# Performance work log

Hardware: AMD Instinct MI355X
Metric: run time of the kernel (lower is better)

## Reference

```python
import jax, jax.numpy as jnp
import numpy as np

N_NODES = 50000
N_EDGES = 1000000
NODE_F = 64
EDGE_F = 64
OUT_F = 128
K = 2  # matches init k=2


def setup_inputs() -> dict:
    key = jax.random.key(0)
    k1, k2, k3, k4, k5, k6 = jax.random.split(key, 6)
    node_feat = jax.random.normal(k1, (N_NODES, NODE_F), dtype=jnp.float32)
    edge_feat = jax.random.normal(k2, (N_EDGES, EDGE_F), dtype=jnp.float32)
    # nn.Linear(edge_feats*2 + node_feats, out_feats): weight [out, in], bias [out]
    W = jax.random.normal(k3, (OUT_F, 2 * EDGE_F + NODE_F), dtype=jnp.float32) * 0.05
    b = jax.random.normal(k4, (OUT_F,), dtype=jnp.float32) * 0.05
    src = jax.random.randint(k5, (N_EDGES,), 0, N_NODES, dtype=jnp.int64)
    dst = jax.random.randint(k6, (N_EDGES,), 0, N_NODES, dtype=jnp.int64)
    return {"node_feat": node_feat, "edge_feat": edge_feat, "W": W, "b": b,
            "src": src, "dst": dst}


def reference(node_feat, edge_feat, W, b, src, dst):
    N = node_feat.shape[0]
    # norm = in_degrees().clamp(min=1) ** -0.5, shape [N, 1]
    deg = jax.ops.segment_sum(jnp.ones_like(dst, dtype=node_feat.dtype), dst,
                              num_segments=N)
    norm = jnp.maximum(deg, 1.0) ** -0.5
    norm = norm[:, None]
    # DGL semantics: update_all(copy_e, sum) overwrites ndata['h'] with the
    # scatter-sum of edge data over destination nodes; apply_edges then copies
    # the (un-normalized) node 'h' back to edges via edge.src.
    e = edge_feat  # [E, EDGE_F]
    fstack = [node_feat]
    for _ in range(K):
        h = jax.ops.segment_sum(e, dst, num_segments=N)  # [N, EDGE_F]
        fstack.append(h * norm)
        e = h[src]  # apply_edges: e = src node h (un-normalized)
    rst = jnp.concatenate(fstack, axis=-1) @ W.T + b  # [N, OUT_F]
    est = rst[src]  # final apply_edges copies lin output to edges
    return rst, est
```

## Files before the change

### kernel.cpp

```cpp
#include <hip/hip_runtime.h>
#include <hip/hip_bf16.h>

#define NF 64
#define N_OUT 128
#define CAT 192
#define CAPL 6
#define CAP 64

typedef __attribute__((ext_vector_type(4))) float f32x4;
typedef __attribute__((ext_vector_type(8))) short bf16x8;

__device__ inline unsigned short f2bf(float x) {
  unsigned u = __float_as_uint(x);
  unsigned r = (u + 0x7fff + ((u >> 16) & 1)) >> 16;
  return (unsigned short)r;
}

__device__ inline ushort4 pack4(f32x4 v) {
  ushort4 r;
  r.x = f2bf(v.x); r.y = f2bf(v.y); r.z = f2bf(v.z); r.w = f2bf(v.w);
  return r;
}

__device__ inline f32x4 unpack4(ushort4 b) {
  f32x4 v;
  v.x = __uint_as_float((unsigned)b.x << 16);
  v.y = __uint_as_float((unsigned)b.y << 16);
  v.z = __uint_as_float((unsigned)b.z << 16);
  v.w = __uint_as_float((unsigned)b.w << 16);
  return v;
}

__device__ inline f32x4 sx4(f32x4 v, int m) {
  f32x4 r;
  r.x = __shfl_xor(v.x, m, 64);
  r.y = __shfl_xor(v.y, m, 64);
  r.z = __shfl_xor(v.z, m, 64);
  r.w = __shfl_xor(v.w, m, 64);
  return r;
}

__global__ __launch_bounds__(256) void fill_kernel(const int* __restrict__ src,
                                                   const int* __restrict__ dst,
                                                   int* __restrict__ cnt,
                                                   long long* __restrict__ bins,
                                                   int n_edges) {
  int i = blockIdx.x * blockDim.x + threadIdx.x;
  if (i >= n_edges) return;
  int d = __builtin_nontemporal_load(&dst[i]);
  int s = __builtin_nontemporal_load(&src[i]);
  int p = atomicAdd(&cnt[d], 1) & (CAP - 1);
  long long pk = (long long)(((unsigned long long)(unsigned)s << 32) | (unsigned)i);
  __builtin_nontemporal_store(pk, &bins[((size_t)d << CAPL) + p]);
}

__global__ __launch_bounds__(256) void h1_kernel(const float* __restrict__ edge_feat,
                                                 const float* __restrict__ node_feat,
                                                 const int2* __restrict__ bins,
                                                 const int* __restrict__ cnt,
                                                 unsigned short* __restrict__ h1r,
                                                 unsigned short* __restrict__ h1n,
                                                 unsigned short* __restrict__ nfb,
                                                 int n_nodes) {
  int n = blockIdx.x * 4 + (threadIdx.x >> 6);
  if (n >= n_nodes) return;
  int l = threadIdx.x & 63;
  int l15 = l & 15, l4 = l >> 4;
  int c = cnt[n];
  if (c > CAP) c = CAP;
  int kb = n << CAPL;
  int ke = kb + c;
  f32x4 acc0 = {0.f,0.f,0.f,0.f}, acc1 = {0.f,0.f,0.f,0.f};
  f32x4 acc2 = {0.f,0.f,0.f,0.f}, acc3 = {0.f,0.f,0.f,0.f};
  int k = kb;
  for (; k + 16 <= ke; k += 16) {
    int e0 = bins[k + l4].x;
    int e1 = bins[k + 4 + l4].x;
    int e2 = bins[k + 8 + l4].x;
    int e3 = bins[k + 12 + l4].x;
    acc0 += __builtin_nontemporal_load((const f32x4*)&edge_feat[(size_t)e0 * NF + l15 * 4]);
    acc1 += __builtin_nontemporal_load((const f32x4*)&edge_feat[(size_t)e1 * NF + l15 * 4]);
    acc2 += __builtin_nontemporal_load((const f32x4*)&edge_feat[(size_t)e2 * NF + l15 * 4]);
    acc3 += __builtin_nontemporal_load((const f32x4*)&edge_feat[(size_t)e3 * NF + l15 * 4]);
  }
  if (k + 8 <= ke) {
    int e0 = bins[k + l4].x;
    int e1 = bins[k + 4 + l4].x;
    acc0 += __builtin_nontemporal_load((const f32x4*)&edge_feat[(size_t)e0 * NF + l15 * 4]);
    acc1 += __builtin_nontemporal_load((const f32x4*)&edge_feat[(size_t)e1 * NF + l15 * 4]);
    k += 8;
  }
  if (k + 4 <= ke) {
    int e = bins[k + l4].x;
    acc2 += __builtin_nontemporal_load((const f32x4*)&edge_feat[(size_t)e * NF + l15 * 4]);
    k += 4;
  }
  int rem = ke - k;
  if (l4 < rem) {
    int e = bins[k + l4].x;
    acc3 += __builtin_nontemporal_load((const f32x4*)&edge_feat[(size_t)e * NF + l15 * 4]);
  }
  f32x4 t = (acc0 + acc1) + (acc2 + acc3);
  t += sx4(t, 16);
  t += sx4(t, 32);
  if (l4 == 0) {
    *(ushort4*)&h1r[(size_t)n * NF + l15 * 4] = pack4(t);
    float nm = rsqrtf(fmaxf((float)c, 1.0f));
    f32x4 tn = t; tn.x *= nm; tn.y *= nm; tn.z *= nm; tn.w *= nm;
    *(ushort4*)&h1n[(size_t)n * NF + l15 * 4] = pack4(tn);
  } else if (l4 == 1) {
    f32x4 v = *(const f32x4*)&node_feat[(size_t)n * NF + l15 * 4];
    *(ushort4*)&nfb[(size_t)n * NF + l15 * 4] = pack4(v);
  }
}

__global__ __launch_bounds__(256) void h2_kernel(const unsigned short* __restrict__ h1r,
                                                 const int2* __restrict__ bins,
                                                 const int* __restrict__ cnt,
                                                 unsigned short* __restrict__ h2n,
                                                 int n_nodes) {
  int n = blockIdx.x * 4 + (threadIdx.x >> 6);
  if (n >= n_nodes) return;
  int l = threadIdx.x & 63;
  int l15 = l & 15, l4 = l >> 4;
  int c = cnt[n];
  if (c > CAP) c = CAP;
  int kb = n << CAPL;
  int ke = kb + c;
  f32x4 acc0 = {0.f,0.f,0.f,0.f}, acc1 = {0.f,0.f,0.f,0.f};
  f32x4 acc2 = {0.f,0.f,0.f,0.f}, acc3 = {0.f,0.f,0.f,0.f};
  int k = kb;
  for (; k + 16 <= ke; k += 16) {
    int s0 = bins[k + l4].y;
    int s1 = bins[k + 4 + l4].y;
    int s2 = bins[k + 8 + l4].y;
    int s3 = bins[k + 12 + l4].y;
    acc0 += unpack4(*(const ushort4*)&h1r[(size_t)s0 * NF + l15 * 4]);
    acc1 += unpack4(*(const ushort4*)&h1r[(size_t)s1 * NF + l15 * 4]);
    acc2 += unpack4(*(const ushort4*)&h1r[(size_t)s2 * NF + l15 * 4]);
    acc3 += unpack4(*(const ushort4*)&h1r[(size_t)s3 * NF + l15 * 4]);
  }
  if (k + 8 <= ke) {
    int s0 = bins[k + l4].y;
    int s1 = bins[k + 4 + l4].y;
    acc0 += unpack4(*(const ushort4*)&h1r[(size_t)s0 * NF + l15 * 4]);
    acc1 += unpack4(*(const ushort4*)&h1r[(size_t)s1 * NF + l15 * 4]);
    k += 8;
  }
  if (k + 4 <= ke) {
    int s = bins[k + l4].y;
    acc2 += unpack4(*(const ushort4*)&h1r[(size_t)s * NF + l15 * 4]);
    k += 4;
  }
  int rem = ke - k;
  if (l4 < rem) {
    int s = bins[k + l4].y;
    acc3 += unpack4(*(const ushort4*)&h1r[(size_t)s * NF + l15 * 4]);
  }
  f32x4 t = (acc0 + acc1) + (acc2 + acc3);
  t += sx4(t, 16);
  t += sx4(t, 32);
  if (l4 == 0) {
    float nm = rsqrtf(fmaxf((float)c, 1.0f));
    t.x *= nm; t.y *= nm; t.z *= nm; t.w *= nm;
    *(ushort4*)&h2n[(size_t)n * NF + l15 * 4] = pack4(t);
  }
}

__global__ __launch_bounds__(512) void gemm_kernel(const unsigned short* __restrict__ nfb,
                                                   const unsigned short* __restrict__ h1n,
                                                   const unsigned short* __restrict__ h2n,
                                                   const float* __restrict__ W,
                                                   const float* __restrict__ bias,
                                                   float* __restrict__ rst,
                                                   unsigned short* __restrict__ rstb,
                                                   int n_nodes) {
  __shared__ short F[64 * 200];
  __shared__ float R[64][132];
  int tid = threadIdx.x;
  int l = tid & 63, w = tid >> 6;
  int w2 = w & 3, wh = w >> 2;
  int l15 = l & 15, l4 = l >> 4;

  bf16x8 Bf[6][2];
  #pragma unroll
  for (int c = 0; c < 2; ++c) {
    int col = w2 * 32 + c * 16 + l15;
    const float* wp = &W[(size_t)col * CAT];
    #pragma unroll
    for (int ks = 0; ks < 6; ++ks) {
      int k0 = ks * 32 + l4 * 8;
      bf16x8 b;
      #pragma unroll
      for (int j = 0; j < 8; ++j) b[j] = (short)f2bf(wp[k0 + j]);
      Bf[ks][c] = b;
    }
  }
  float bias0 = bias[w2 * 32 + l15];
  float bias1 = bias[w2 * 32 + 16 + l15];

  int tiles = (n_nodes + 63) / 64;
  for (int tile = blockIdx.x; tile < tiles; tile += gridDim.x) {
    int nbase = tile * 64;
    __syncthreads();
    for (int idx = tid; idx < 1536; idx += 512) {
      int m = idx / 24, q = idx - m * 24;
      int n = nbase + m;
      bf16x8 pk = bf16x8{0,0,0,0,0,0,0,0};
      if (n < n_nodes) {
        const unsigned short* base = (q < 8) ? nfb : (q < 16) ? h1n : h2n;
        pk = *(const bf16x8*)&base[(size_t)n * NF + (q & 7) * 8];
      }
      *(bf16x8*)&F[m * 200 + q * 8] = pk;
    }
    __syncthreads();
    f32x4 acc00 = {0.f,0.f,0.f,0.f}, acc01 = {0.f,0.f,0.f,0.f};
    f32x4 acc10 = {0.f,0.f,0.f,0.f}, acc11 = {0.f,0.f,0.f,0.f};
    #pragma unroll
    for (int ks = 0; ks < 6; ++ks) {
      bf16x8 a0 = *(const bf16x8*)&F[(wh * 32 + l15) * 200 + ks * 32 + l4 * 8];
      bf16x8 a1 = *(const bf16x8*)&F[(wh * 32 + 16 + l15) * 200 + ks * 32 + l4 * 8];
      acc00 = __builtin_amdgcn_mfma_f32_16x16x32_bf16(a0, Bf[ks][0], acc00, 0, 0, 0);
      acc01 = __builtin_amdgcn_mfma_f32_16x16x32_bf16(a0, Bf[ks][1], acc01, 0, 0, 0);
      acc10 = __builtin_amdgcn_mfma_f32_16x16x32_bf16(a1, Bf[ks][0], acc10, 0, 0, 0);
      acc11 = __builtin_amdgcn_mfma_f32_16x16x32_bf16(a1, Bf[ks][1], acc11, 0, 0, 0);
    }
    #pragma unroll
    for (int rt = 0; rt < 2; ++rt) {
      f32x4 ac0 = rt ? acc10 : acc00;
      f32x4 ac1 = rt ? acc11 : acc01;
      #pragma unroll
      for (int r = 0; r < 4; ++r) {
        int row = wh * 32 + rt * 16 + l4 * 4 + r;
        R[row][w2 * 32 + l15] = ac0[r] + bias0;
        R[row][w2 * 32 + 16 + l15] = ac1[r] + bias1;
      }
    }
    __syncthreads();
    for (int idx = tid; idx < 64 * 32; idx += 512) {
      int m = idx >> 5, c = idx & 31;
      int n = nbase + m;
      if (n < n_nodes) {
        f32x4 v = *(const f32x4*)&R[m][c * 4];
        __builtin_nontemporal_store(v, (f32x4*)&rst[(size_t)n * N_OUT + c * 4]);
      }
    }
    for (int idx = tid; idx < 64 * 16; idx += 512) {
      int m = idx >> 4, q = idx & 15;
      int n = nbase + m;
      if (n < n_nodes) {
        const float* rp = &R[m][q * 8];
        bf16x8 pk;
        #pragma unroll
        for (int j = 0; j < 8; ++j) pk[j] = (short)f2bf(rp[j]);
        *(bf16x8*)&rstb[(size_t)n * N_OUT + q * 8] = pk;
      }
    }
  }
}

__global__ __launch_bounds__(256) void est_bf16_kernel(const unsigned short* __restrict__ rstb,
                                                       const int* __restrict__ src,
                                                       float* __restrict__ est, int n_edges) {
  f32x4* e4 = (f32x4*)est;
  int total = n_edges * 32;
  int i = blockIdx.x * blockDim.x + threadIdx.x;
  int stride = gridDim.x * blockDim.x;
  for (; i < total; i += stride) {
    int e = i >> 5, c = i & 31;
    ushort4 b = *(const ushort4*)&rstb[(size_t)src[e] * N_OUT + c * 4];
    __builtin_nontemporal_store(unpack4(b), &e4[i]);
  }
}

extern "C" void kernel_launch(void* const* d_in, const int* in_sizes, int n_in,
                              void* d_out, int out_size, void* d_ws, size_t ws_size,
                              hipStream_t stream) {
  const float* node_feat = (const float*)d_in[0];
  const float* edge_feat = (const float*)d_in[1];
  const float* W = (const float*)d_in[2];
  const float* bias = (const float*)d_in[3];
  const int* src = (const int*)d_in[4];
  const int* dst = (const int*)d_in[5];
  int n_nodes = in_sizes[0] / NF;
  int n_edges = in_sizes[4];

  size_t off = 0;
  auto take = [&](size_t bytes) -> void* {
    void* p = (char*)d_ws + off;
    off += (bytes + 255) & ~(size_t)255;
    return p;
  };
  int* cnt = (int*)take((size_t)n_nodes * 4);
  long long* bins = (long long*)take((size_t)n_nodes * CAP * 8);
  unsigned short* h1r = (unsigned short*)take((size_t)n_nodes * NF * 2);
  unsigned short* h1n = (unsigned short*)take((size_t)n_nodes * NF * 2);
  unsigned short* h2n = (unsigned short*)take((size_t)n_nodes * NF * 2);
  unsigned short* nfb = (unsigned short*)take((size_t)n_nodes * NF * 2);
  unsigned short* rstb = (unsigned short*)take((size_t)n_nodes * N_OUT * 2);

  float* rst = (float*)d_out;
  float* est = rst + (size_t)n_nodes * N_OUT;

  (void)hipMemsetAsync(cnt, 0, (size_t)n_nodes * 4, stream);

  fill_kernel<<<(n_edges + 255) / 256, 256, 0, stream>>>(src, dst, cnt, bins, n_edges);
  int nb = (n_nodes + 3) / 4;
  h1_kernel<<<nb, 256, 0, stream>>>(edge_feat, node_feat, (const int2*)bins, cnt,
                                    h1r, h1n, nfb, n_nodes);
  h2_kernel<<<nb, 256, 0, stream>>>(h1r, (const int2*)bins, cnt, h2n, n_nodes);
  gemm_kernel<<<512, 512, 0, stream>>>(nfb, h1n, h2n, W, bias, rst, rstb, n_nodes);
  est_bf16_kernel<<<8192, 256, 0, stream>>>(rstb, src, est, n_edges);
}
```

Baseline: 326.1 us.

## Replace per-node atomic binning with chunked counting sort into 64-node buckets

Swaps the per-destination global-atomic fill (64 slots per node) for a three-pass counting sort: per-chunk LDS histograms over 64-node buckets, a wave-level prefix scan, and a placement pass using LDS atomics. The h1/h2 aggregation kernels now process one 64-node bucket per block, accumulating gathered rows into a shared-memory tile with LDS float atomics and computing degree on the fly. This removes the global atomics and memset and gives more regular writes, but adds two extra launches, serialised 64-block count/place passes, and LDS atomic contention. It also caps each bucket at 2048 edges, so overflow is silently dropped.

Measured after the change: 1.051 ms. 222% more time.

```diff
diff --git a/kernel.cpp b/kernel.cpp
--- a/kernel.cpp
+++ b/kernel.cpp
@@ -4,8 +4,9 @@
 #define NF 64
 #define N_OUT 128
 #define CAT 192
-#define CAPL 6
-#define CAP 64
+#define BCAP 2048
+#define NCHUNK 64
+#define MAXB 800
 
 typedef __attribute__((ext_vector_type(4))) float f32x4;
 typedef __attribute__((ext_vector_type(8))) short bf16x8;
@@ -31,139 +32,169 @@
   return v;
 }
 
-__device__ inline f32x4 sx4(f32x4 v, int m) {
-  f32x4 r;
-  r.x = __shfl_xor(v.x, m, 64);
-  r.y = __shfl_xor(v.y, m, 64);
-  r.z = __shfl_xor(v.z, m, 64);
-  r.w = __shfl_xor(v.w, m, 64);
-  return r;
-}
-
-__global__ __launch_bounds__(256) void fill_kernel(const int* __restrict__ src,
-                                                   const int* __restrict__ dst,
-                                                   int* __restrict__ cnt,
-                                                   long long* __restrict__ bins,
-                                                   int n_edges) {
-  int i = blockIdx.x * blockDim.x + threadIdx.x;
-  if (i >= n_edges) return;
-  int d = __builtin_nontemporal_load(&dst[i]);
-  int s = __builtin_nontemporal_load(&src[i]);
-  int p = atomicAdd(&cnt[d], 1) & (CAP - 1);
-  long long pk = (long long)(((unsigned long long)(unsigned)s << 32) | (unsigned)i);
-  __builtin_nontemporal_store(pk, &bins[((size_t)d << CAPL) + p]);
+__global__ __launch_bounds__(1024) void count_kernel(const int* __restrict__ dst,
+                                                     int* __restrict__ count,
+                                                     int n_edges, int nb) {
+  __shared__ int hist[MAXB];
+  int tid = threadIdx.x;
+  for (int i = tid; i < nb; i += 1024) hist[i] = 0;
+  __syncthreads();
+  int chunk = (n_edges + NCHUNK - 1) / NCHUNK;
+  int beg = blockIdx.x * chunk;
+  int end = min(beg + chunk, n_edges);
+  for (int i = beg + tid; i < end; i += 1024) {
+    int d = __builtin_nontemporal_load(&dst[i]);
+    atomicAdd(&hist[d >> 6], 1);
+  }
+  __syncthreads();
+  for (int b = tid; b < nb; b += 1024) count[b * NCHUNK + blockIdx.x] = hist[b];
+}
+
+__global__ __launch_bounds__(256) void scan_kernel(int* __restrict__ count,
+                                                   int* __restrict__ total, int nb) {
+  int tid = threadIdx.x;
+  int b = blockIdx.x * 4 + (tid >> 6);
+  int l = tid & 63;
+  if (b >= nb) return;
+  int c = count[b * NCHUNK + l];
+  int c8 = (c + 7) & ~7;
+  int s = c8;
+  #pragma unroll
+  for (int o = 1; o < 64; o <<= 1) {
+    int t = __shfl_up(s, o, 64);
+    if (l >= o) s += t;
+  }
+  count[b * NCHUNK + l] = s - c8;
+  if (l == 63) total[b] = s;
+}
+
+__global__ __launch_bounds__(1024) void place_kernel(const int* __restrict__ src,
+                                                     const int* __restrict__ dst,
+                                                     const int* __restrict__ count,
+                                                     long long* __restrict__ bins,
+                                                     int n_edges, int nb) {
+  __shared__ int lbase[MAXB], lrank[MAXB];
+  int tid = threadIdx.x;
+  for (int i = tid; i < nb; i += 1024) {
+    lbase[i] = count[i * NCHUNK + blockIdx.x];
+    lrank[i] = 0;
+  }
+  __syncthreads();
+  int chunk = (n_edges + NCHUNK - 1) / NCHUNK;
+  int beg = blockIdx.x * chunk;
+  int end = min(beg + chunk, n_edges);
+  for (int i = beg + tid; i < end; i += 1024) {
+    int d = __builtin_nontemporal_load(&dst[i]);
+    int s = __builtin_nontemporal_load(&src[i]);
+    int b = d >> 6;
+    int r = atomicAdd(&lrank[b], 1);
+    int pos = lbase[b] + r;
+    if (pos < BCAP) {
+      long long pk = ((long long)(unsigned)s << 32) |
+                     (unsigned)(i | ((d & 63) << 20));
+      bins[(size_t)b * BCAP + pos] = pk;
+    }
+  }
+  __syncthreads();
+  for (int b = tid; b < nb; b += 1024) {
+    int r = lbase[b] + lrank[b];
+    int r8 = (r + 7) & ~7;
+    for (; r < r8 && r < BCAP; ++r) bins[(size_t)b * BCAP + r] = -1LL;
+  }
 }
 
 __global__ __launch_bounds__(256) void h1_kernel(const float* __restrict__ edge_feat,
                                                  const float* __restrict__ node_feat,
-                                                 const int2* __restrict__ bins,
-                                                 const int* __restrict__ cnt,
+                                                 const long long* __restrict__ bins,
+                                                 const int* __restrict__ total,
                                                  unsigned short* __restrict__ h1r,
                                                  unsigned short* __restrict__ h1n,
                                                  unsigned short* __restrict__ nfb,
                                                  int n_nodes) {
-  int n = blockIdx.x * 4 + (threadIdx.x >> 6);
-  if (n >= n_nodes) return;
-  int l = threadIdx.x & 63;
-  int l15 = l & 15, l4 = l >> 4;
-  int c = cnt[n];
-  if (c > CAP) c = CAP;
-  int kb = n << CAPL;
-  int ke = kb + c;
-  f32x4 acc0 = {0.f,0.f,0.f,0.f}, acc1 = {0.f,0.f,0.f,0.f};
-  f32x4 acc2 = {0.f,0.f,0.f,0.f}, acc3 = {0.f,0.f,0.f,0.f};
-  int k = kb;
-  for (; k + 16 <= ke; k += 16) {
-    int e0 = bins[k + l4].x;
-    int e1 = bins[k + 4 + l4].x;
-    int e2 = bins[k + 8 + l4].x;
-    int e3 = bins[k + 12 + l4].x;
-    acc0 += __builtin_nontemporal_load((const f32x4*)&edge_feat[(size_t)e0 * NF + l15 * 4]);
-    acc1 += __builtin_nontemporal_load((const f32x4*)&edge_feat[(size_t)e1 * NF + l15 * 4]);
-    acc2 += __builtin_nontemporal_load((const f32x4*)&edge_feat[(size_t)e2 * NF + l15 * 4]);
-    acc3 += __builtin_nontemporal_load((const f32x4*)&edge_feat[(size_t)e3 * NF + l15 * 4]);
-  }
-  if (k + 8 <= ke) {
-    int e0 = bins[k + l4].x;
-    int e1 = bins[k + 4 + l4].x;
-    acc0 += __builtin_nontemporal_load((const f32x4*)&edge_feat[(size_t)e0 * NF + l15 * 4]);
-    acc1 += __builtin_nontemporal_load((const f32x4*)&edge_feat[(size_t)e1 * NF + l15 * 4]);
-    k += 8;
-  }
-  if (k + 4 <= ke) {
-    int e = bins[k + l4].x;
-    acc2 += __builtin_nontemporal_load((const f32x4*)&edge_feat[(size_t)e * NF + l15 * 4]);
-    k += 4;
-  }
-  int rem = ke - k;
-  if (l4 < rem) {
-    int e = bins[k + l4].x;
-    acc3 += __builtin_nontemporal_load((const f32x4*)&edge_feat[(size_t)e * NF + l15 * 4]);
-  }
-  f32x4 t = (acc0 + acc1) + (acc2 + acc3);
-  t += sx4(t, 16);
-  t += sx4(t, 32);
-  if (l4 == 0) {
-    *(ushort4*)&h1r[(size_t)n * NF + l15 * 4] = pack4(t);
-    float nm = rsqrtf(fmaxf((float)c, 1.0f));
-    f32x4 tn = t; tn.x *= nm; tn.y *= nm; tn.z *= nm; tn.w *= nm;
-    *(ushort4*)&h1n[(size_t)n * NF + l15 * 4] = pack4(tn);
-  } else if (l4 == 1) {
-    f32x4 v = *(const f32x4*)&node_feat[(size_t)n * NF + l15 * 4];
-    *(ushort4*)&nfb[(size_t)n * NF + l15 * 4] = pack4(v);
+  __shared__ float acc[64][68];
+  __shared__ int deg[64];
+  int tid = threadIdx.x;
+  int b = blockIdx.x;
+  int nbase = b << 6;
+  for (int i = tid; i < 64 * 64; i += 256) acc[i >> 6][i & 63] = 0.f;
+  if (tid < 64) deg[tid] = 0;
+  __syncthreads();
+  int tot = total[b];
+  if (tot > BCAP) tot = BCAP;
+  int l15 = tid & 15, grp = tid >> 4;
+  const long long* bb = &bins[(size_t)b * BCAP];
+  for (int k = grp; k < tot; k += 16) {
+    long long pk = bb[k];
+    int lo = (int)pk;
+    if (lo == -1) continue;
+    int e = lo & 0xFFFFF;
+    int row = (lo >> 20) & 63;
+    f32x4 v = __builtin_nontemporal_load((const f32x4*)&edge_feat[(size_t)e * NF + l15 * 4]);
+    atomicAdd(&acc[row][l15 * 4 + 0], v.x);
+    atomicAdd(&acc[row][l15 * 4 + 1], v.y);
+    atomicAdd(&acc[row][l15 * 4 + 2], v.z);
+    atomicAdd(&acc[row][l15 * 4 + 3], v.w);
+    if (l15 == 0) atomicAdd(&deg[row], 1);
+  }
+  __syncthreads();
+  for (int idx = tid; idx < 64 * 16; idx += 256) {
+    int m = idx >> 4, q = idx & 15;
+    int n = nbase + m;
+    if (n >= n_nodes) continue;
+    f32x4 t;
+    t.x = acc[m][q * 4 + 0]; t.y = acc[m][q * 4 + 1];
+    t.z = acc[m][q * 4 + 2]; t.w = acc[m][q * 4 + 3];
+    *(ushort4*)&h1r[(size_t)n * NF + q * 4] = pack4(t);
+    float nm = rsqrtf(fmaxf((float)deg[m], 1.0f));
+    f32x4 tn = t;
+    tn.x *= nm; tn.y *= nm; tn.z *= nm; tn.w *= nm;
+    *(ushort4*)&h1n[(size_t)n * NF + q * 4] = pack4(tn);
+    f32x4 v = *(const f32x4*)&node_feat[(size_t)n * NF + q * 4];
+    *(ushort4*)&nfb[(size_t)n * NF + q * 4] = pack4(v);
   }
 }
 
 __global__ __launch_bounds__(256) void h2_kernel(const unsigned short* __restrict__ h1r,
-                                                 const int2* __restrict__ bins,
-                                                 const int* __restrict__ cnt,
+                                                 const long long* __restrict__ bins,
+                                                 const int* __restrict__ total,
                                                  unsigned short* __restrict__ h2n,
                                                  int n_nodes) {
-  int n = blockIdx.x * 4 + (threadIdx.x >> 6);
-  if (n >= n_nodes) return;
-  int l = threadIdx.x & 63;
-  int l15 = l & 15, l4 = l >> 4;
-  int c = cnt[n];
-  if (c > CAP) c = CAP;
-  int kb = n << CAPL;
-  int ke = kb + c;
-  f32x4 acc0 = {0.f,0.f,0.f,0.f}, acc1 = {0.f,0.f,0.f,0.f};
-  f32x4 acc2 = {0.f,0.f,0.f,0.f}, acc3 = {0.f,0.f,0.f,0.f};
-  int k = kb;
-  for (; k + 16 <= ke; k += 16) {
-    int s0 = bins[k + l4].y;
-    int s1 = bins[k + 4 + l4].y;
-    int s2 = bins[k + 8 + l4].y;
-    int s3 = bins[k + 12 + l4].y;
-    acc0 += unpack4(*(const ushort4*)&h1r[(size_t)s0 * NF + l15 * 4]);
-    acc1 += unpack4(*(const ushort4*)&h1r[(size_t)s1 * NF + l15 * 4]);
-    acc2 += unpack4(*(const ushort4*)&h1r[(size_t)s2 * NF + l15 * 4]);
-    acc3 += unpack4(*(const ushort4*)&h1r[(size_t)s3 * NF + l15 * 4]);
-  }
-  if (k + 8 <= ke) {
-    int s0 = bins[k + l4].y;
-    int s1 = bins[k + 4 + l4].y;
-    acc0 += unpack4(*(const ushort4*)&h1r[(size_t)s0 * NF + l15 * 4]);
-    acc1 += unpack4(*(const ushort4*)&h1r[(size_t)s1 * NF + l15 * 4]);
-    k += 8;
-  }
-  if (k + 4 <= ke) {
-    int s = bins[k + l4].y;
-    acc2 += unpack4(*(const ushort4*)&h1r[(size_t)s * NF + l15 * 4]);
-    k += 4;
-  }
-  int rem = ke - k;
-  if (l4 < rem) {
-    int s = bins[k + l4].y;
-    acc3 += unpack4(*(const ushort4*)&h1r[(size_t)s * NF + l15 * 4]);
-  }
-  f32x4 t = (acc0 + acc1) + (acc2 + acc3);
-  t += sx4(t, 16);
-  t += sx4(t, 32);
-  if (l4 == 0) {
-    float nm = rsqrtf(fmaxf((float)c, 1.0f));
+  __shared__ float acc[64][68];
+  __shared__ int deg[64];
+  int tid = threadIdx.x;
+  int b = blockIdx.x;
+  int nbase = b << 6;
+  for (int i = tid; i < 64 * 64; i += 256) acc[i >> 6][i & 63] = 0.f;
+  if (tid < 64) deg[tid] = 0;
+  __syncthreads();
+  int tot = total[b];
+  if (tot > BCAP) tot = BCAP;
+  int l15 = tid & 15, grp = tid >> 4;
+  const long long* bb = &bins[(size_t)b * BCAP];
+  for (int k = grp; k < tot; k += 16) {
+    long long pk = bb[k];
+    int lo = (int)pk;
+    if (lo == -1) continue;
+    int s = (int)(pk >> 32);
+    int row = (lo >> 20) & 63;
+    f32x4 v = unpack4(*(const ushort4*)&h1r[(size_t)s * NF + l15 * 4]);
+    atomicAdd(&acc[row][l15 * 4 + 0], v.x);
+    atomicAdd(&acc[row][l15 * 4 + 1], v.y);
+    atomicAdd(&acc[row][l15 * 4 + 2], v.z);
+    atomicAdd(&acc[row][l15 * 4 + 3], v.w);
+    if (l15 == 0) atomicAdd(&deg[row], 1);
+  }
+  __syncthreads();
+  for (int idx = tid; idx < 64 * 16; idx += 256) {
+    int m = idx >> 4, q = idx & 15;
+    int n = nbase + m;
+    if (n >= n_nodes) continue;
+    f32x4 t;
+    t.x = acc[m][q * 4 + 0]; t.y = acc[m][q * 4 + 1];
+    t.z = acc[m][q * 4 + 2]; t.w = acc[m][q * 4 + 3];
+    float nm = rsqrtf(fmaxf((float)deg[m], 1.0f));
     t.x *= nm; t.y *= nm; t.z *= nm; t.w *= nm;
-    *(ushort4*)&h2n[(size_t)n * NF + l15 * 4] = pack4(t);
+    *(ushort4*)&h2n[(size_t)n * NF + q * 4] = pack4(t);
   }
 }
 
@@ -284,6 +315,7 @@
   const int* dst = (const int*)d_in[5];
   int n_nodes = in_sizes[0] / NF;
   int n_edges = in_sizes[4];
+  int nb = (n_nodes + 63) >> 6;
 
   size_t off = 0;
   auto take = [&](size_t bytes) -> void* {
@@ -291,8 +323,9 @@
     off += (bytes + 255) & ~(size_t)255;
     return p;
   };
-  int* cnt = (int*)take((size_t)n_nodes * 4);
-  long long* bins = (long long*)take((size_t)n_nodes * CAP * 8);
+  int* count = (int*)take((size_t)nb * NCHUNK * 4);
+  int* total = (int*)take((size_t)nb * 4);
+  long long* bins = (long long*)take((size_t)nb * BCAP * 8);
   unsigned short* h1r = (unsigned short*)take((size_t)n_nodes * NF * 2);
   unsigned short* h1n = (unsigned short*)take((size_t)n_nodes * NF * 2);
   unsigned short* h2n = (unsigned short*)take((size_t)n_nodes * NF * 2);
@@ -302,13 +335,12 @@
   float* rst = (float*)d_out;
   float* est = rst + (size_t)n_nodes * N_OUT;
 
-  (void)hipMemsetAsync(cnt, 0, (size_t)n_nodes * 4, stream);
-
-  fill_kernel<<<(n_edges + 255) / 256, 256, 0, stream>>>(src, dst, cnt, bins, n_edges);
-  int nb = (n_nodes + 3) / 4;
-  h1_kernel<<<nb, 256, 0, stream>>>(edge_feat, node_feat, (const int2*)bins, cnt,
+  count_kernel<<<NCHUNK, 1024, 0, stream>>>(dst, count, n_edges, nb);
+  scan_kernel<<<(nb + 3) / 4, 256, 0, stream>>>(count, total, nb);
+  place_kernel<<<NCHUNK, 1024, 0, stream>>>(src, dst, count, bins, n_edges, nb);
+  h1_kernel<<<nb, 256, 0, stream>>>(edge_feat, node_feat, bins, total,
                                     h1r, h1n, nfb, n_nodes);
-  h2_kernel<<<nb, 256, 0, stream>>>(h1r, (const int2*)bins, cnt, h2n, n_nodes);
+  h2_kernel<<<nb, 256, 0, stream>>>(h1r, bins, total, h2n, n_nodes);
   gemm_kernel<<<512, 512, 0, stream>>>(nfb, h1n, h2n, W, bias, rst, rstb, n_nodes);
   est_bf16_kernel<<<8192, 256, 0, stream>>>(rstb, src, est, n_edges);
 }
```
